# Kernel optimization log

Hardware: AMD Instinct MI355X
Metric: run time of the kernel (lower is better)

## Reference

```python
import jax, jax.numpy as jnp
import numpy as np


def setup_inputs() -> dict:
    key = jax.random.key(0)
    k0, k1, k2, k3 = jax.random.split(key, 4)
    B, T, D, F, E = 4, 2048, 512, 1024, 8
    x = jax.random.normal(k0, (B, T, D), dtype=jnp.float32)
    # router weight is zero-init in the original; use small random values so top-k
    router_w = 0.02 * jax.random.normal(k1, (E, D), dtype=jnp.float32)
    router_b = jnp.zeros((E,), dtype=jnp.float32)
    w_gate_up = 0.02 * jax.random.normal(k2, (E, D, 2 * F), dtype=jnp.float32)
    w_down = 0.02 * jax.random.normal(k3, (E, F, D), dtype=jnp.float32)
    return {"x": x, "router_w": router_w, "router_b": router_b,
            "w_gate_up": w_gate_up, "w_down": w_down, "top_k": 2}


def reference(x, router_w, router_b, w_gate_up, w_down, top_k):
    B, T, D = x.shape
    E = router_w.shape[0]
    x_flat = x.reshape(-1, D)                      # [N, D]
    N = x_flat.shape[0]

    # router: softmax over experts, top-k, renormalize
    logits = x_flat @ router_w.T + router_b       # [N, E]
    probs = jax.nn.softmax(logits, axis=-1)
    top_w, top_idx = jax.lax.top_k(probs, top_k)  # [N, k]
    top_w = top_w / jnp.sum(top_w, axis=-1, keepdims=True)

    # scatter renormalized weights into a dense [N, E] combine matrix
    combine = jnp.zeros((N, E), dtype=x.dtype).at[
        jnp.arange(N)[:, None], top_idx].add(top_w)

    # per-expert SwiGLU; combine weights zero out non-selected experts, giving
    # math identical to the sort/gather/scatter dispatch in the original
    out = jnp.zeros_like(x_flat)
    for e in range(E):  # fixed small expert count, not a data-dim loop
        gate_up = x_flat @ w_gate_up[e]           # [N, 2F]
        gate, up = jnp.split(gate_up, 2, axis=-1)
        h = jax.nn.silu(gate) * up                # [N, F]
        out = out + combine[:, e:e + 1] * (h @ w_down[e])
    return out.reshape(B, T, D)
```

## Files before the change

### kernel.cpp

```cpp
#include <hip/hip_runtime.h>
#include <stdint.h>

#define N_TOK 8192
#define D_DIM 512
#define F_DIM 1024
#define E_NUM 8
#define M_SLOTS (N_TOK * 2)

typedef __bf16 bf16x8 __attribute__((ext_vector_type(8)));
typedef float f32x4 __attribute__((ext_vector_type(4)));

__device__ __forceinline__ ushort f2b(float f) {
    union { float f; unsigned u; } v; v.f = f;
    unsigned r = v.u + 0x7fffu + ((v.u >> 16) & 1u);
    return (ushort)(r >> 16);
}
__device__ __forceinline__ float b2f(ushort u) {
    union { unsigned i; float f; } v; v.i = ((unsigned)u) << 16; return v.f;
}
__device__ __forceinline__ void gload16(const void* g, void* l) {
    __builtin_amdgcn_global_load_lds(
        (const __attribute__((address_space(1))) unsigned int*)g,
        (__attribute__((address_space(3))) unsigned int*)l, 16, 0, 0);
}

__global__ __launch_bounds__(256) void pre_k(const float* __restrict__ x,
                                             const float* __restrict__ rw,
                                             const float* __restrict__ rb,
                                             ushort* __restrict__ x_bf,
                                             int* __restrict__ tok_e,
                                             float* __restrict__ tok_w,
                                             int* __restrict__ cnt,
                                             const float* __restrict__ wgu,
                                             ushort* __restrict__ wgu_t,
                                             const float* __restrict__ wd,
                                             ushort* __restrict__ wd_t) {
    __shared__ ushort tile[64][65];
    int b = blockIdx.x;
    if (b < N_TOK / 4) {
        if (b == 0 && threadIdx.x < 16) cnt[threadIdx.x] = 0;
        int lane = threadIdx.x & 63, wv = threadIdx.x >> 6;
        int t = b * 4 + wv;
        float4 xa = *(const float4*)(x + (size_t)t * D_DIM + lane * 8);
        float4 xb = *(const float4*)(x + (size_t)t * D_DIM + lane * 8 + 4);
        ushort u[8] = {f2b(xa.x), f2b(xa.y), f2b(xa.z), f2b(xa.w),
                       f2b(xb.x), f2b(xb.y), f2b(xb.z), f2b(xb.w)};
        *(uint4*)(x_bf + (size_t)t * D_DIM + lane * 8) = *(const uint4*)u;

        float acc[E_NUM];
#pragma unroll
        for (int e = 0; e < E_NUM; ++e) {
            float4 wa = *(const float4*)(rw + (size_t)e * D_DIM + lane * 8);
            float4 wb = *(const float4*)(rw + (size_t)e * D_DIM + lane * 8 + 4);
            float s = xa.x * wa.x + xa.y * wa.y + xa.z * wa.z + xa.w * wa.w +
                      xb.x * wb.x + xb.y * wb.y + xb.z * wb.z + xb.w * wb.w;
#pragma unroll
            for (int o = 32; o > 0; o >>= 1) s += __shfl_xor(s, o, 64);
            acc[e] = s;
        }
        if (lane == 0) {
            float l[E_NUM];
#pragma unroll
            for (int e = 0; e < E_NUM; ++e) l[e] = acc[e] + rb[e];
            int e0 = 0;
#pragma unroll
            for (int e = 1; e < E_NUM; ++e) if (l[e] > l[e0]) e0 = e;
            int e1 = (e0 == 0) ? 1 : 0;
#pragma unroll
            for (int e = 0; e < E_NUM; ++e) if (e != e0 && l[e] > l[e1]) e1 = e;
            float p1 = __expf(l[e1] - l[e0]);
            float w0 = 1.f / (1.f + p1), w1 = p1 / (1.f + p1);
            tok_e[2 * t] = e0;  tok_e[2 * t + 1] = e1;
            tok_w[2 * t] = w0;  tok_w[2 * t + 1] = w1;
        }
        return;
    }
    int tb = b - N_TOK / 4;
    const float* src; ushort* dst; int R, C, c0, r0;
    if (tb < 2048) {
        int e = tb >> 8, rem = tb & 255;
        R = D_DIM; C = 2 * F_DIM;
        src = wgu + (size_t)e * R * C; dst = wgu_t + (size_t)e * R * C;
        c0 = (rem & 31) * 64; r0 = (rem >> 5) * 64;
    } else {
        int b2 = tb - 2048;
        int e = b2 >> 7, rem = b2 & 127;
        R = F_DIM; C = D_DIM;
        src = wd + (size_t)e * R * C; dst = wd_t + (size_t)e * R * C;
        c0 = (rem & 7) * 64; r0 = (rem >> 3) * 64;
    }
#pragma unroll
    for (int i = 0; i < 4; ++i) {
        int ch = threadIdx.x + i * 256;
        int row = ch >> 4, pos = ch & 15;
        float4 v = *(const float4*)(src + (size_t)(r0 + row) * C + c0 + pos * 4);
        tile[row][pos * 4 + 0] = f2b(v.x);
        tile[row][pos * 4 + 1] = f2b(v.y);
        tile[row][pos * 4 + 2] = f2b(v.z);
        tile[row][pos * 4 + 3] = f2b(v.w);
    }
    __syncthreads();
#pragma unroll
    for (int i = 0; i < 2; ++i) {
        int ch = threadIdx.x + i * 256;
        int ocol = ch >> 3, rb_ = ch & 7;
        ushort tmp[8];
#pragma unroll
        for (int j = 0; j < 8; ++j) tmp[j] = tile[rb_ * 8 + j][ocol];
        *(uint4*)(dst + (size_t)(c0 + ocol) * R + r0 + rb_ * 8) = *(const uint4*)tmp;
    }
}

__global__ __launch_bounds__(256) void assign_k(const int* __restrict__ tok_e,
                                                int* __restrict__ cnt,
                                                int* __restrict__ rank) {
    __shared__ int lcnt[E_NUM], lbase[E_NUM];
    int tid = threadIdx.x;
    int i = blockIdx.x * 256 + tid;
    if (tid < E_NUM) lcnt[tid] = 0;
    __syncthreads();
    int e = tok_e[i];
    int intra = atomicAdd(&lcnt[e], 1);
    __syncthreads();
    if (tid < E_NUM) lbase[tid] = atomicAdd(&cnt[tid], lcnt[tid]);
    __syncthreads();
    rank[i] = lbase[e] + intra;
}

__global__ __launch_bounds__(256) void scatter_k(const int* __restrict__ tok_e,
                                                 const int* __restrict__ rank,
                                                 const int* __restrict__ cnt,
                                                 int* __restrict__ ebase,
                                                 int* __restrict__ row_token,
                                                 int* __restrict__ tok_pos) {
    __shared__ int eb[E_NUM];
    int tid = threadIdx.x;
    if (tid == 0) {
        int s = 0;
        for (int k = 0; k < E_NUM; ++k) {
            eb[k] = s;
            if (blockIdx.x == 0) ebase[k] = s;
            s += cnt[k];
        }
        if (blockIdx.x == 0) ebase[E_NUM] = s;
    }
    __syncthreads();
    int i = blockIdx.x * 256 + tid;
    int pos = eb[tok_e[i]] + rank[i];
    row_token[pos] = i >> 1;
    tok_pos[i] = pos;
}

__global__ __launch_bounds__(256, 3) void gemm1_k(const ushort* __restrict__ x,
                                                  const ushort* __restrict__ wgu_t,
                                                  const int* __restrict__ ebase,
                                                  const int* __restrict__ row_token,
                                                  ushort* __restrict__ h) {
    int e = blockIdx.z;
    int base = ebase[e];
    int cnt = ebase[e + 1] - base;
    int tile0 = blockIdx.y * 128;
    if (tile0 >= cnt) return;
    int c0 = blockIdx.x * 64;

    __shared__ __align__(16) ushort smem[3 * 8192];

    int tid = threadIdx.x;
    int lane = tid & 63, wv = tid >> 6;
    int wr = wv >> 1, wc = wv & 1;

    const ushort* asrc[2];
    const ushort* bsrc[2];
#pragma unroll
    for (int i = 0; i < 2; ++i) {
        int c = tid + i * 256;
        int rp = c >> 3, s = c & 7;
        int lp = s ^ (rp & 7);
        int row = 2 * rp + (lp >> 2);
        int q = lp & 3;
        int r = tile0 + row;
        r = (r < cnt) ? r : (cnt - 1);
        int tok = row_token[base + r];
        asrc[i] = x + (size_t)tok * D_DIM + q * 8;
        int gc = (row < 64) ? (c0 + row) : (F_DIM + c0 + row - 64);
        bsrc[i] = wgu_t + ((size_t)e * (2 * F_DIM) + gc) * D_DIM + q * 8;
    }

    f32x4 accg[4][2], accu[4][2];
#pragma unroll
    for (int a = 0; a < 4; ++a)
#pragma unroll
        for (int b = 0; b < 2; ++b) {
            accg[a][b] = (f32x4){0.f, 0.f, 0.f, 0.f};
            accu[a][b] = (f32x4){0.f, 0.f, 0.f, 0.f};
        }

    int q = lane >> 4, m = lane & 15;
    int mh = m >> 1;
    int sl = (4 * (m & 1) + q) ^ (mh & 7);
    int soff = sl * 8;

    auto stage = [&](ushort* buf, int kk) {
#pragma unroll
        for (int i = 0; i < 2; ++i) {
            int c = tid + i * 256;
            gload16(asrc[i] + kk, buf + (size_t)c * 8);
            gload16(bsrc[i] + kk, buf + 4096 + (size_t)c * 8);
        }
    };
    auto compute = [&](const ushort* la_) {
        const ushort* lb_ = la_ + 4096;
        bf16x8 af[4], bg[2], bu[2];
#pragma unroll
        for (int mt = 0; mt < 4; ++mt)
            af[mt] = *(const bf16x8*)(la_ + (wr * 32 + mt * 8 + mh) * 64 + soff);
#pragma unroll
        for (int nt = 0; nt < 2; ++nt) {
            bg[nt] = *(const bf16x8*)(lb_ + (wc * 16 + nt * 8 + mh) * 64 + soff);
            bu[nt] = *(const bf16x8*)(lb_ + (32 + wc * 16 + nt * 8 + mh) * 64 + soff);
        }
#pragma unroll
        for (int mt = 0; mt < 4; ++mt)
#pragma unroll
            for (int nt = 0; nt < 2; ++nt) {
                accg[mt][nt] = __builtin_amdgcn_mfma_f32_16x16x32_bf16(af[mt], bg[nt], accg[mt][nt], 0, 0, 0);
                accu[mt][nt] = __builtin_amdgcn_mfma_f32_16x16x32_bf16(af[mt], bu[nt], accu[mt][nt], 0, 0, 0);
            }
    };

    ushort* pc = smem;
    ushort* pn = smem + 8192;
    ushort* pf = smem + 16384;

    stage(pc, 0);
    stage(pn, 32);
    asm volatile("s_waitcnt vmcnt(4) lgkmcnt(0)" ::: "memory");
    __builtin_amdgcn_s_barrier();
    __builtin_amdgcn_sched_barrier(0);

    for (int k = 64; k <= D_DIM - 32; k += 32) {
        stage(pf, k);
        compute(pc);
        asm volatile("s_waitcnt vmcnt(4) lgkmcnt(0)" ::: "memory");
        __builtin_amdgcn_s_barrier();
        __builtin_amdgcn_sched_barrier(0);
        ushort* t_ = pc; pc = pn; pn = pf; pf = t_;
    }
    compute(pc);
    asm volatile("s_waitcnt vmcnt(0) lgkmcnt(0)" ::: "memory");
    __builtin_amdgcn_s_barrier();
    __builtin_amdgcn_sched_barrier(0);
    compute(pn);

    __syncthreads();
    ushort* stg = smem;
#pragma unroll
    for (int mt = 0; mt < 4; ++mt)
#pragma unroll
        for (int nt = 0; nt < 2; ++nt) {
            int sc = wc * 32 + nt * 16 + m;
#pragma unroll
            for (int r4 = 0; r4 < 4; ++r4) {
                int rr = wr * 64 + mt * 16 + q * 4 + r4;
                float g = accg[mt][nt][r4];
                float u = accu[mt][nt][r4];
                stg[rr * 68 + sc] = f2b((g / (1.f + __expf(-g))) * u);
            }
        }
    __syncthreads();
#pragma unroll
    for (int p = 0; p < 4; ++p) {
        int c = tid + p * 256;
        int sr = c >> 3, coff = (c & 7) * 8;
        int grow = tile0 + sr;
        if (grow < cnt)
            *(uint4*)(h + (size_t)(base + grow) * F_DIM + c0 + coff) =
                *(const uint4*)(stg + sr * 68 + coff);
    }
}

__global__ __launch_bounds__(256, 3) void gemm2_k(const ushort* __restrict__ h,
                                                  const ushort* __restrict__ wd_t,
                                                  const int* __restrict__ ebase,
                                                  ushort* __restrict__ slot) {
    int e = blockIdx.z;
    int base = ebase[e];
    int cnt = ebase[e + 1] - base;
    int tile0 = blockIdx.y * 128;
    if (tile0 >= cnt) return;
    int c0 = blockIdx.x * 128;

    __shared__ __align__(16) ushort smem[3 * 8192];

    int tid = threadIdx.x;
    int lane = tid & 63, wv = tid >> 6;
    int wr = wv >> 1, wc = wv & 1;

    const ushort* asrc[2]; const ushort* bsrc[2];
#pragma unroll
    for (int i = 0; i < 2; ++i) {
        int c = tid + i * 256;
        int rp = c >> 3, s = c & 7;
        int lp = s ^ (rp & 7);
        int row = 2 * rp + (lp >> 2);
        int q = lp & 3;
        int r = tile0 + row;
        r = (r < cnt) ? r : (cnt - 1);
        asrc[i] = h + (size_t)(base + r) * F_DIM + q * 8;
        bsrc[i] = wd_t + ((size_t)e * D_DIM + c0 + row) * F_DIM + q * 8;
    }

    f32x4 acc[4][4];
#pragma unroll
    for (int a = 0; a < 4; ++a)
#pragma unroll
        for (int b = 0; b < 4; ++b) acc[a][b] = (f32x4){0.f, 0.f, 0.f, 0.f};

    int q = lane >> 4, m = lane & 15;
    int mh = m >> 1;
    int sl = (4 * (m & 1) + q) ^ (mh & 7);
    int soff = sl * 8;

    auto stage = [&](ushort* buf, int kk) {
#pragma unroll
        for (int i = 0; i < 2; ++i) {
            int c = tid + i * 256;
            gload16(asrc[i] + kk, buf + (size_t)c * 8);
            gload16(bsrc[i] + kk, buf + 4096 + (size_t)c * 8);
        }
    };
    auto compute = [&](const ushort* la_) {
        const ushort* lb_ = la_ + 4096;
        bf16x8 af[4], bb[4];
#pragma unroll
        for (int mt = 0; mt < 4; ++mt)
            af[mt] = *(const bf16x8*)(la_ + (wr * 32 + mt * 8 + mh) * 64 + soff);
#pragma unroll
        for (int nt = 0; nt < 4; ++nt)
            bb[nt] = *(const bf16x8*)(lb_ + (wc * 32 + nt * 8 + mh) * 64 + soff);
        __builtin_amdgcn_s_setprio(1);
#pragma unroll
        for (int mt = 0; mt < 4; ++mt)
#pragma unroll
            for (int nt = 0; nt < 4; ++nt)
                acc[mt][nt] = __builtin_amdgcn_mfma_f32_16x16x32_bf16(af[mt], bb[nt], acc[mt][nt], 0, 0, 0);
        __builtin_amdgcn_s_setprio(0);
    };

    ushort* pc = smem;
    ushort* pn = smem + 8192;
    ushort* pf = smem + 16384;

    stage(pc, 0);
    stage(pn, 32);
    asm volatile("s_waitcnt vmcnt(4) lgkmcnt(0)" ::: "memory");
    __builtin_amdgcn_s_barrier();
    __builtin_amdgcn_sched_barrier(0);

    for (int k = 64; k <= F_DIM - 32; k += 32) {
        stage(pf, k);
        compute(pc);
        asm volatile("s_waitcnt vmcnt(4) lgkmcnt(0)" ::: "memory");
        __builtin_amdgcn_s_barrier();
        __builtin_amdgcn_sched_barrier(0);
        ushort* t_ = pc; pc = pn; pn = pf; pf = t_;
    }
    compute(pc);
    asm volatile("s_waitcnt vmcnt(0) lgkmcnt(0)" ::: "memory");
    __builtin_amdgcn_s_barrier();
    __builtin_amdgcn_sched_barrier(0);
    compute(pn);

    __syncthreads();
    ushort* stg = smem;
#pragma unroll
    for (int mt = 0; mt < 4; ++mt)
#pragma unroll
        for (int nt = 0; nt < 4; ++nt) {
            int scol = wc * 64 + nt * 16 + m;
#pragma unroll
            for (int r4 = 0; r4 < 4; ++r4) {
                int rr = wr * 64 + mt * 16 + q * 4 + r4;
                stg[rr * 132 + scol] = f2b(acc[mt][nt][r4]);
            }
        }
    __syncthreads();
#pragma unroll
    for (int p = 0; p < 8; ++p) {
        int c = tid + p * 256;
        int sr = c >> 4, coff = (c & 15) * 8;
        int grow = tile0 + sr;
        if (grow < cnt)
            *(uint4*)(slot + (size_t)(base + grow) * D_DIM + c0 + coff) =
                *(const uint4*)(stg + sr * 132 + coff);
    }
}

__global__ __launch_bounds__(256) void combine_k(const ushort* __restrict__ slot,
                                                 const int* __restrict__ tok_pos,
                                                 const float* __restrict__ tok_w,
                                                 float* __restrict__ out) {
    int lane = threadIdx.x & 63, wv = threadIdx.x >> 6;
    int t = blockIdx.x * 4 + wv;
    int p0 = tok_pos[2 * t], p1 = tok_pos[2 * t + 1];
    float w0 = tok_w[2 * t], w1 = tok_w[2 * t + 1];
    uint4 s0 = *(const uint4*)(slot + (size_t)p0 * D_DIM + lane * 8);
    uint4 s1 = *(const uint4*)(slot + (size_t)p1 * D_DIM + lane * 8);
    const ushort* a = (const ushort*)&s0;
    const ushort* b = (const ushort*)&s1;
    float o[8];
#pragma unroll
    for (int j = 0; j < 8; ++j) o[j] = w0 * b2f(a[j]) + w1 * b2f(b[j]);
    float* dst = out + (size_t)t * D_DIM + lane * 8;
    *(float4*)dst = (float4){o[0], o[1], o[2], o[3]};
    *(float4*)(dst + 4) = (float4){o[4], o[5], o[6], o[7]};
}

extern "C" void kernel_launch(void* const* d_in, const int* in_sizes, int n_in,
                              void* d_out, int out_size, void* d_ws, size_t ws_size,
                              hipStream_t stream) {
    const float* x   = (const float*)d_in[0];
    const float* rw  = (const float*)d_in[1];
    const float* rb  = (const float*)d_in[2];
    const float* wgu = (const float*)d_in[3];
    const float* wd  = (const float*)d_in[4];
    float* out = (float*)d_out;

    char* ws = (char*)d_ws;
    size_t off = 0;
    auto alloc = [&](size_t bytes) -> void* {
        void* p = ws + off;
        off += (bytes + 255) & ~(size_t)255;
        return p;
    };
    ushort* wgu_t     = (ushort*)alloc((size_t)E_NUM * 2 * F_DIM * D_DIM * 2);
    ushort* wd_t      = (ushort*)alloc((size_t)E_NUM * D_DIM * F_DIM * 2);
    ushort* x_bf      = (ushort*)alloc((size_t)N_TOK * D_DIM * 2);
    ushort* hbuf      = (ushort*)alloc((size_t)M_SLOTS * F_DIM * 2);
    ushort* slot      = (ushort*)alloc((size_t)M_SLOTS * D_DIM * 2);
    int*    row_token = (int*)alloc(M_SLOTS * 4);
    int*    tok_e     = (int*)alloc(M_SLOTS * 4);
    int*    rankbuf   = (int*)alloc(M_SLOTS * 4);
    float*  tok_w     = (float*)alloc(M_SLOTS * 4);
    int*    tok_pos   = (int*)alloc(M_SLOTS * 4);
    int*    cnt       = (int*)alloc(64);
    int*    ebase     = (int*)alloc(64);

    pre_k<<<N_TOK / 4 + 3072, 256, 0, stream>>>(x, rw, rb, x_bf, tok_e, tok_w, cnt,
                                                wgu, wgu_t, wd, wd_t);
    assign_k<<<M_SLOTS / 256, 256, 0, stream>>>(tok_e, cnt, rankbuf);
    scatter_k<<<M_SLOTS / 256, 256, 0, stream>>>(tok_e, rankbuf, cnt, ebase, row_token, tok_pos);
    gemm1_k<<<dim3(16, 32, E_NUM), 256, 0, stream>>>(x_bf, wgu_t, ebase, row_token, hbuf);
    gemm2_k<<<dim3(4, 32, E_NUM), 256, 0, stream>>>(hbuf, wd_t, ebase, slot);
    combine_k<<<N_TOK / 4, 256, 0, stream>>>(slot, tok_pos, tok_w, out);
}
```

Baseline: 204.6 us.

## Compact MoE GEMM grids via tile map and split LDS fragment loads from MFMA

Builds a compact tile map in the scatter kernel so the expert GEMM grids launch only about 136 live row tiles instead of 32x8, with early exit for padded entries. This removes launching and retiring many empty blocks and makes the order in which live tiles are scheduled more uniform. It also splits the inner loop into a fragment-load phase and an MFMA phase with an extra barrier, and adds setprio in gemm1. The extra barrier per k-step may add synchronization cost.

```diff
diff --git a/kernel.cpp b/kernel.cpp
--- a/kernel.cpp
+++ b/kernel.cpp
@@ -6,6 +6,7 @@
 #define F_DIM 1024
 #define E_NUM 8
 #define M_SLOTS (N_TOK * 2)
+#define NTILE_MAX 136
 
 typedef __bf16 bf16x8 __attribute__((ext_vector_type(8)));
 typedef float f32x4 __attribute__((ext_vector_type(4)));
@@ -132,7 +133,8 @@
                                                  const int* __restrict__ cnt,
                                                  int* __restrict__ ebase,
                                                  int* __restrict__ row_token,
-                                                 int* __restrict__ tok_pos) {
+                                                 int* __restrict__ tok_pos,
+                                                 int* __restrict__ tmap) {
     __shared__ int eb[E_NUM];
     int tid = threadIdx.x;
     if (tid == 0) {
@@ -142,7 +144,14 @@
             if (blockIdx.x == 0) ebase[k] = s;
             s += cnt[k];
         }
-        if (blockIdx.x == 0) ebase[E_NUM] = s;
+        if (blockIdx.x == 0) {
+            ebase[E_NUM] = s;
+            int idx = 0;
+            for (int k = 0; k < E_NUM; ++k)
+                for (int t0 = 0; t0 * 128 < cnt[k]; ++t0)
+                    tmap[idx++] = (k << 16) | t0;
+            for (; idx < NTILE_MAX; ++idx) tmap[idx] = -1;
+        }
     }
     __syncthreads();
     int i = blockIdx.x * 256 + tid;
@@ -155,12 +164,14 @@
                                                   const ushort* __restrict__ wgu_t,
                                                   const int* __restrict__ ebase,
                                                   const int* __restrict__ row_token,
+                                                  const int* __restrict__ tmap,
                                                   ushort* __restrict__ h) {
-    int e = blockIdx.z;
+    int tm = tmap[blockIdx.y];
+    if (tm < 0) return;
+    int e = tm >> 16;
+    int tile0 = (tm & 0xffff) * 128;
     int base = ebase[e];
     int cnt = ebase[e + 1] - base;
-    int tile0 = blockIdx.y * 128;
-    if (tile0 >= cnt) return;
     int c0 = blockIdx.x * 64;
 
     __shared__ __align__(16) ushort smem[3 * 8192];
@@ -200,6 +211,7 @@
     int sl = (4 * (m & 1) + q) ^ (mh & 7);
     int soff = sl * 8;
 
+    bf16x8 af[4], bg[2], bu[2];
     auto stage = [&](ushort* buf, int kk) {
 #pragma unroll
         for (int i = 0; i < 2; ++i) {
@@ -208,9 +220,8 @@
             gload16(bsrc[i] + kk, buf + 4096 + (size_t)c * 8);
         }
     };
-    auto compute = [&](const ushort* la_) {
+    auto load_frags = [&](const ushort* la_) {
         const ushort* lb_ = la_ + 4096;
-        bf16x8 af[4], bg[2], bu[2];
 #pragma unroll
         for (int mt = 0; mt < 4; ++mt)
             af[mt] = *(const bf16x8*)(la_ + (wr * 32 + mt * 8 + mh) * 64 + soff);
@@ -219,6 +230,9 @@
             bg[nt] = *(const bf16x8*)(lb_ + (wc * 16 + nt * 8 + mh) * 64 + soff);
             bu[nt] = *(const bf16x8*)(lb_ + (32 + wc * 16 + nt * 8 + mh) * 64 + soff);
         }
+    };
+    auto do_mfma = [&]() {
+        __builtin_amdgcn_s_setprio(1);
 #pragma unroll
         for (int mt = 0; mt < 4; ++mt)
 #pragma unroll
@@ -226,6 +240,7 @@
                 accg[mt][nt] = __builtin_amdgcn_mfma_f32_16x16x32_bf16(af[mt], bg[nt], accg[mt][nt], 0, 0, 0);
                 accu[mt][nt] = __builtin_amdgcn_mfma_f32_16x16x32_bf16(af[mt], bu[nt], accu[mt][nt], 0, 0, 0);
             }
+        __builtin_amdgcn_s_setprio(0);
     };
 
     ushort* pc = smem;
@@ -240,17 +255,27 @@
 
     for (int k = 64; k <= D_DIM - 32; k += 32) {
         stage(pf, k);
-        compute(pc);
-        asm volatile("s_waitcnt vmcnt(4) lgkmcnt(0)" ::: "memory");
+        load_frags(pc);
+        __builtin_amdgcn_s_barrier();
+        asm volatile("s_waitcnt lgkmcnt(0)" ::: "memory");
+        __builtin_amdgcn_sched_barrier(0);
+        do_mfma();
+        asm volatile("s_waitcnt vmcnt(4)" ::: "memory");
         __builtin_amdgcn_s_barrier();
         __builtin_amdgcn_sched_barrier(0);
         ushort* t_ = pc; pc = pn; pn = pf; pf = t_;
     }
-    compute(pc);
+    load_frags(pc);
+    asm volatile("s_waitcnt lgkmcnt(0)" ::: "memory");
+    __builtin_amdgcn_sched_barrier(0);
+    do_mfma();
     asm volatile("s_waitcnt vmcnt(0) lgkmcnt(0)" ::: "memory");
     __builtin_amdgcn_s_barrier();
     __builtin_amdgcn_sched_barrier(0);
-    compute(pn);
+    load_frags(pn);
+    asm volatile("s_waitcnt lgkmcnt(0)" ::: "memory");
+    __builtin_amdgcn_sched_barrier(0);
+    do_mfma();
 
     __syncthreads();
     ushort* stg = smem;
@@ -282,12 +307,14 @@
 __global__ __launch_bounds__(256, 3) void gemm2_k(const ushort* __restrict__ h,
                                                   const ushort* __restrict__ wd_t,
                                                   const int* __restrict__ ebase,
+                                                  const int* __restrict__ tmap,
                                                   ushort* __restrict__ slot) {
-    int e = blockIdx.z;
+    int tm = tmap[blockIdx.y];
+    if (tm < 0) return;
+    int e = tm >> 16;
+    int tile0 = (tm & 0xffff) * 128;
     int base = ebase[e];
     int cnt = ebase[e + 1] - base;
-    int tile0 = blockIdx.y * 128;
-    if (tile0 >= cnt) return;
     int c0 = blockIdx.x * 128;
 
     __shared__ __align__(16) ushort smem[3 * 8192];
@@ -321,6 +348,7 @@
     int sl = (4 * (m & 1) + q) ^ (mh & 7);
     int soff = sl * 8;
 
+    bf16x8 af[4], bb[4];
     auto stage = [&](ushort* buf, int kk) {
 #pragma unroll
         for (int i = 0; i < 2; ++i) {
@@ -329,15 +357,16 @@
             gload16(bsrc[i] + kk, buf + 4096 + (size_t)c * 8);
         }
     };
-    auto compute = [&](const ushort* la_) {
+    auto load_frags = [&](const ushort* la_) {
         const ushort* lb_ = la_ + 4096;
-        bf16x8 af[4], bb[4];
 #pragma unroll
         for (int mt = 0; mt < 4; ++mt)
             af[mt] = *(const bf16x8*)(la_ + (wr * 32 + mt * 8 + mh) * 64 + soff);
 #pragma unroll
         for (int nt = 0; nt < 4; ++nt)
             bb[nt] = *(const bf16x8*)(lb_ + (wc * 32 + nt * 8 + mh) * 64 + soff);
+    };
+    auto do_mfma = [&]() {
         __builtin_amdgcn_s_setprio(1);
 #pragma unroll
         for (int mt = 0; mt < 4; ++mt)
@@ -359,17 +388,27 @@
 
     for (int k = 64; k <= F_DIM - 32; k += 32) {
         stage(pf, k);
-        compute(pc);
-        asm volatile("s_waitcnt vmcnt(4) lgkmcnt(0)" ::: "memory");
+        load_frags(pc);
+        __builtin_amdgcn_s_barrier();
+        asm volatile("s_waitcnt lgkmcnt(0)" ::: "memory");
+        __builtin_amdgcn_sched_barrier(0);
+        do_mfma();
+        asm volatile("s_waitcnt vmcnt(4)" ::: "memory");
         __builtin_amdgcn_s_barrier();
         __builtin_amdgcn_sched_barrier(0);
         ushort* t_ = pc; pc = pn; pn = pf; pf = t_;
     }
-    compute(pc);
+    load_frags(pc);
+    asm volatile("s_waitcnt lgkmcnt(0)" ::: "memory");
+    __builtin_amdgcn_sched_barrier(0);
+    do_mfma();
     asm volatile("s_waitcnt vmcnt(0) lgkmcnt(0)" ::: "memory");
     __builtin_amdgcn_s_barrier();
     __builtin_amdgcn_sched_barrier(0);
-    compute(pn);
+    load_frags(pn);
+    asm volatile("s_waitcnt lgkmcnt(0)" ::: "memory");
+    __builtin_amdgcn_sched_barrier(0);
+    do_mfma();
 
     __syncthreads();
     ushort* stg = smem;
@@ -445,12 +484,14 @@
     int*    tok_pos   = (int*)alloc(M_SLOTS * 4);
     int*    cnt       = (int*)alloc(64);
     int*    ebase     = (int*)alloc(64);
+    int*    tmap      = (int*)alloc(NTILE_MAX * 4);
 
     pre_k<<<N_TOK / 4 + 3072, 256, 0, stream>>>(x, rw, rb, x_bf, tok_e, tok_w, cnt,
                                                 wgu, wgu_t, wd, wd_t);
     assign_k<<<M_SLOTS / 256, 256, 0, stream>>>(tok_e, cnt, rankbuf);
-    scatter_k<<<M_SLOTS / 256, 256, 0, stream>>>(tok_e, rankbuf, cnt, ebase, row_token, tok_pos);
-    gemm1_k<<<dim3(16, 32, E_NUM), 256, 0, stream>>>(x_bf, wgu_t, ebase, row_token, hbuf);
-    gemm2_k<<<dim3(4, 32, E_NUM), 256, 0, stream>>>(hbuf, wd_t, ebase, slot);
+    scatter_k<<<M_SLOTS / 256, 256, 0, stream>>>(tok_e, rankbuf, cnt, ebase,
+                                                 row_token, tok_pos, tmap);
+    gemm1_k<<<dim3(16, NTILE_MAX), 256, 0, stream>>>(x_bf, wgu_t, ebase, row_token, tmap, hbuf);
+    gemm2_k<<<dim3(4, NTILE_MAX), 256, 0, stream>>>(hbuf, wd_t, ebase, tmap, slot);
     combine_k<<<N_TOK / 4, 256, 0, stream>>>(slot, tok_pos, tok_w, out);
 }
```

Result: no change. 207.0 us (+1.2%).
